# Optimization experiments

Measured on AMD Instinct MI355X. Metric: run time of the kernel, lower is better.

## Reference

```python
import jax, jax.numpy as jnp
import numpy as np

HID_DIM = 1024
B, S = 8, 2048
SCALE = float(np.sqrt(HID_DIM))
NEG = -1e10


def setup_inputs() -> dict:
    key = jax.random.key(0)
    ks = jax.random.split(key, 13)
    d = HID_DIM
    std = 1.0 / np.sqrt(d)
    return {
        "query": jax.random.normal(ks[0], (B, S, d), jnp.float32),
        "key_": jax.random.normal(ks[1], (B, S, d), jnp.float32),
        "value": jax.random.normal(ks[2], (B, S, d), jnp.float32),
        "mask": jax.random.randint(ks[3], (B, S), 0, 2, jnp.int32),
        "Wq": jax.random.uniform(ks[4], (d, d), jnp.float32, -std, std),
        "bq": jax.random.uniform(ks[5], (d,), jnp.float32, -std, std),
        "Wk": jax.random.uniform(ks[6], (d, d), jnp.float32, -std, std),
        "bk": jax.random.uniform(ks[7], (d,), jnp.float32, -std, std),
        "Wv": jax.random.uniform(ks[8], (d, d), jnp.float32, -std, std),
        "bv": jax.random.uniform(ks[9], (d,), jnp.float32, -std, std),
        "Wfc": jax.random.uniform(ks[10], (d, d), jnp.float32, -std, std),
        "bfc": jax.random.uniform(ks[11], (d,), jnp.float32, -std, std),
    }


def reference(query, key_, value, mask, Wq, bq, Wk, bk, Wv, bv, Wfc, bfc):
    # Linear projections (torch Linear: x @ W.T + b)
    Q = jnp.einsum("bsd,ed->bse", query, Wq) + bq
    K = jnp.einsum("bsd,ed->bse", key_, Wk) + bk
    V = jnp.einsum("bsd,ed->bse", value, Wv) + bv
    # Scaled dot-product energy: [B, S, S]
    energy = jnp.einsum("bqd,bkd->bqk", Q, K) / SCALE
    # Faithful to source: mask broadcast over last dim masks QUERY rows
    energy = jnp.where(mask[:, :, None] == 0, NEG, energy)
    attention = jax.nn.softmax(energy, axis=-1)  # dropout=0 (eval)
    x = jnp.einsum("bqk,bkd->bqd", attention, V)
    out = jnp.einsum("bsd,ed->bse", x, Wfc) + bfc
    return out
```

## Files before the change

kernel.cpp:

```cpp
#include <hip/hip_runtime.h>
#include <hip/hip_bf16.h>


#define DEVINL __device__ __forceinline__

typedef __bf16 bf16x8 __attribute__((ext_vector_type(8)));
typedef float f32x4 __attribute__((ext_vector_type(4)));

static constexpr int Bb = 8;
static constexpr int S = 2048;
static constexpr int D = 1024;

DEVINL unsigned short f32_to_bf16(float f) {
  unsigned u = __float_as_uint(f);
  u = (u + 0x7FFFu + ((u >> 16) & 1u)) >> 16;
  return (unsigned short)u;
}
DEVINL float bflo(unsigned u) { return __uint_as_float(u << 16); }
DEVINL float bfhi(unsigned u) { return __uint_as_float(u & 0xFFFF0000u); }

DEVINL void gload16(const unsigned short* g, char* l) {
  __builtin_amdgcn_global_load_lds((__attribute__((address_space(1))) void*)g,
                                   (__attribute__((address_space(3))) void*)l,
                                   16, 0, 0);
}
DEVINL void gload16u(const unsigned short* g, unsigned short* l) {
  gload16(g, (char*)l);
}

#define BAR() __builtin_amdgcn_s_barrier()
#define LGK0() asm volatile("s_waitcnt lgkmcnt(0)" ::: "memory")

#define PH_OPEN() \
  BAR();          \
  LGK0();         \
  __builtin_amdgcn_s_setprio(1)
#define PH_CLOSE()               \
  __builtin_amdgcn_s_setprio(0); \
  BAR()

#define MFMA_QUAD(A_, B_, MO, NO)                                              \
  {                                                                            \
    _Pragma("unroll") for (int mi_ = 0; mi_ < 4; mi_++) {                      \
      _Pragma("unroll") for (int nj_ = 0; nj_ < 2; nj_++) {                    \
        acc[(MO) + mi_][(NO) + nj_] = __builtin_amdgcn_mfma_f32_16x16x32_bf16( \
            A_[mi_][0], B_[nj_][0], acc[(MO) + mi_][(NO) + nj_], 0, 0, 0);     \
        acc[(MO) + mi_][(NO) + nj_] = __builtin_amdgcn_mfma_f32_16x16x32_bf16( \
            A_[mi_][1], B_[nj_][1], acc[(MO) + mi_][(NO) + nj_], 0, 0, 0);     \
      }                                                                        \
    }                                                                          \
  }

__global__ __launch_bounds__(256) void conv_f32_bf16(const float* __restrict__ in,
                                                     unsigned short* __restrict__ out,
                                                     int n8) {
  int i = blockIdx.x * 256 + threadIdx.x;
  int stride = gridDim.x * 256;
  for (; i < n8; i += stride) {
    const float4* p = (const float4*)in + (size_t)i * 2;
    float4 a = p[0], b = p[1];
    uint4 o;
    o.x = (unsigned)f32_to_bf16(a.x) | ((unsigned)f32_to_bf16(a.y) << 16);
    o.y = (unsigned)f32_to_bf16(a.z) | ((unsigned)f32_to_bf16(a.w) << 16);
    o.z = (unsigned)f32_to_bf16(b.x) | ((unsigned)f32_to_bf16(b.y) << 16);
    o.w = (unsigned)f32_to_bf16(b.z) | ((unsigned)f32_to_bf16(b.w) << 16);
    ((uint4*)out)[i] = o;
  }
}

__global__ __launch_bounds__(256) void tconv(const float* __restrict__ in,
                                             unsigned short* __restrict__ out,
                                             int R, int C) {
  __shared__ unsigned short t[64][72];
  const int c0 = blockIdx.x * 64, r0 = blockIdx.y * 64, b = blockIdx.z;
  in += (size_t)b * R * C;
  out += (size_t)b * R * C;
  const int tr = threadIdx.x >> 4;
  const int tc = threadIdx.x & 15;
#pragma unroll
  for (int i = 0; i < 4; i++) {
    int row = tr + i * 16;
    float4 v = *(const float4*)(in + (size_t)(r0 + row) * C + c0 + tc * 4);
    t[tc * 4 + 0][row] = f32_to_bf16(v.x);
    t[tc * 4 + 1][row] = f32_to_bf16(v.y);
    t[tc * 4 + 2][row] = f32_to_bf16(v.z);
    t[tc * 4 + 3][row] = f32_to_bf16(v.w);
  }
  __syncthreads();
  const int c = threadIdx.x >> 2, rs = (threadIdx.x & 3) * 16;
  unsigned short tmp[16];
#pragma unroll
  for (int j = 0; j < 16; j++) tmp[j] = t[c][rs + j];
  *(uint4*)(out + (size_t)(c0 + c) * R + r0 + rs) = *(const uint4*)&tmp[0];
  *(uint4*)(out + (size_t)(c0 + c) * R + r0 + rs + 8) = *(const uint4*)&tmp[8];
}

__global__ __launch_bounds__(256) void cvec_kernel(const float* __restrict__ Wfc,
                                                   const float* __restrict__ bv,
                                                   const float* __restrict__ bfc,
                                                   float* __restrict__ cv) {
  const int f = blockIdx.x;
  const float* row = Wfc + (size_t)f * 1024;
  float s = 0.f;
  for (int e = threadIdx.x; e < 1024; e += 256) s += row[e] * bv[e];
#pragma unroll
  for (int off = 32; off >= 1; off >>= 1) s += __shfl_xor(s, off);
  __shared__ float red[4];
  const int wave = threadIdx.x >> 6, lane = threadIdx.x & 63;
  if (lane == 0) red[wave] = s;
  __syncthreads();
  if (threadIdx.x == 0) cv[f] = red[0] + red[1] + red[2] + red[3] + bfc[f];
}

__global__ __launch_bounds__(256) void gvec_kernel(const unsigned short* __restrict__ WkT,
                                                   const float* __restrict__ bq,
                                                   float* __restrict__ g32) {
  const int e = blockIdx.x;
  const unsigned short* row = WkT + (size_t)e * 1024;
  const int j0 = threadIdx.x * 4;
  uint2 v = *(const uint2*)(row + j0);
  float4 b4 = *(const float4*)(bq + j0);
  float s = bflo(v.x) * b4.x + bfhi(v.x) * b4.y + bflo(v.y) * b4.z + bfhi(v.y) * b4.w;
#pragma unroll
  for (int off = 32; off >= 1; off >>= 1) s += __shfl_xor(s, off);
  __shared__ float red[4];
  const int wave = threadIdx.x >> 6, lane = threadIdx.x & 63;
  if (lane == 0) red[wave] = s;
  __syncthreads();
  if (threadIdx.x == 0) g32[e] = (red[0] + red[1] + red[2] + red[3]) * (1.0f / 32.0f);
}

__global__ __launch_bounds__(256) void wvec_kernel(const unsigned short* __restrict__ xk,
                                                   const float* __restrict__ g32,
                                                   float* __restrict__ w32) {
  const int row = blockIdx.x * 4 + (threadIdx.x >> 6);
  const int lane = threadIdx.x & 63;
  const unsigned short* r = xk + (size_t)row * 1024;
  float s = 0.f;
#pragma unroll
  for (int c = 0; c < 2; c++) {
    const int e0 = c * 512 + lane * 8;
    uint4 v = *(const uint4*)(r + e0);
    unsigned u[4] = {v.x, v.y, v.z, v.w};
#pragma unroll
    for (int i = 0; i < 4; i++) {
      float2 gg = *(const float2*)(g32 + e0 + i * 2);
      s += bflo(u[i]) * gg.x + bfhi(u[i]) * gg.y;
    }
  }
#pragma unroll
  for (int off = 32; off >= 1; off >>= 1) s += __shfl_xor(s, off);
  if (lane == 0) w32[row] = s;
}

__global__ __launch_bounds__(256) void rowinv_kernel(const float* __restrict__ partialT,
                                                     float* __restrict__ rowinv) {
  const int r = blockIdx.x * 256 + threadIdx.x;
  float s = 0.f;
#pragma unroll
  for (int c = 0; c < 16; c++) s += partialT[(size_t)c * 16384 + r];
  rowinv[r] = 1.0f / s;
}

__global__ __launch_bounds__(256) void gemm128(const unsigned short* __restrict__ A,
                                               const unsigned short* __restrict__ Bt,
                                               unsigned short* __restrict__ C,
                                               int M, int N, int K,
                                               long long bsA, long long bsB, long long bsC) {
  const int tid = threadIdx.x;
  const int wave = tid >> 6;
  const int lane = tid & 63;
  const int wr = wave >> 1, wc = wave & 1;
  const int m0 = blockIdx.y * 128, n0 = blockIdx.x * 128;
  A += (size_t)blockIdx.z * bsA;
  Bt += (size_t)blockIdx.z * bsB;
  C += (size_t)blockIdx.z * bsC;

  __shared__ unsigned short lds[2][2][128 * 32];

  const int srow = wave * 16 + (lane >> 2);
  const int scol = (lane & 3) * 8;
  const unsigned short* gA = A + (size_t)(m0 + srow) * K + scol;
  const unsigned short* gB = Bt + (size_t)(n0 + srow) * K + scol;

  f32x4 acc[4][4];
#pragma unroll
  for (int i = 0; i < 4; i++)
#pragma unroll
    for (int j = 0; j < 4; j++) acc[i][j] = (f32x4){0.f, 0.f, 0.f, 0.f};

  const int nk = K >> 5;
  auto stage = [&](int buf, int kt) {
    const unsigned short* a0 = gA + (size_t)kt * 32;
    const unsigned short* b0 = gB + (size_t)kt * 32;
    unsigned short* la = &lds[buf][0][wave * 512];
    unsigned short* lb = &lds[buf][1][wave * 512];
    gload16u(a0, la);
    gload16u(a0 + (size_t)64 * K, la + 2048);
    gload16u(b0, lb);
    gload16u(b0 + (size_t)64 * K, lb + 2048);
  };

  stage(0, 0);
  asm volatile("s_waitcnt vmcnt(0)" ::: "memory");
  __syncthreads();

  const int fm = lane & 15;
  const int fk = (lane >> 4) * 8;

  int cur = 0;
  for (int t = 0; t < nk; ++t) {
    if (t + 1 < nk) stage(cur ^ 1, t + 1);
    bf16x8 af[4], bfr[4];
#pragma unroll
    for (int i = 0; i < 4; i++)
      af[i] = *(const bf16x8*)&lds[cur][0][(wr * 64 + i * 16 + fm) * 32 + fk];
#pragma unroll
    for (int j = 0; j < 4; j++)
      bfr[j] = *(const bf16x8*)&lds[cur][1][(wc * 64 + j * 16 + fm) * 32 + fk];
#pragma unroll
    for (int i = 0; i < 4; i++)
#pragma unroll
      for (int j = 0; j < 4; j++)
        acc[i][j] = __builtin_amdgcn_mfma_f32_16x16x32_bf16(af[i], bfr[j], acc[i][j], 0, 0, 0);
    asm volatile("s_waitcnt vmcnt(0)" ::: "memory");
    __syncthreads();
    cur ^= 1;
  }

  const int en = n0 + wc * 64 + fm;
  const int em = m0 + wr * 64 + ((lane >> 4) << 2);
#pragma unroll
  for (int j = 0; j < 4; j++)
#pragma unroll
    for (int i = 0; i < 4; i++)
#pragma unroll
      for (int r = 0; r < 4; r++)
        C[(size_t)(em + i * 16 + r) * N + en + j * 16] = f32_to_bf16(acc[i][j][r]);
}

template <int OUTMODE, bool HAS_BIAS>
__global__ __launch_bounds__(512, 2) void gemm256(
    const unsigned short* __restrict__ A, const unsigned short* __restrict__ Bt,
    const float* __restrict__ bias, const int* __restrict__ msk,
    float* __restrict__ partial, void* __restrict__ Cv,
    int M, int N, int K, long long bsA, long long bsB, long long bsC,
    float scale) {
  extern __shared__ char smem[];
  const int tid = threadIdx.x;
  const int wave = tid >> 6, lane = tid & 63;
  const int wr = wave >> 2, wc = wave & 3;

  const int gx = gridDim.x, gy = gridDim.y;
  const int nwg = gx * gy * (int)gridDim.z;
  const int wg = blockIdx.x + gx * (blockIdx.y + gy * blockIdx.z);
  const int swz = (wg & 7) * (nwg >> 3) + (wg >> 3);
  const int bx = swz % gx;
  const int rem = swz / gx;
  const int by = rem % gy;
  const int bz = rem / gy;

  const int m0 = by * 256, n0 = bx * 256;
  A += (size_t)bz * bsA;
  Bt += (size_t)bz * bsB;

  const int rl = lane >> 3;
  const int gl = (lane & 7) ^ rl;
  const unsigned short* gA = A + (size_t)(m0 + wave * 8 + rl) * K + gl * 8;
  const unsigned short* gB = Bt + (size_t)(n0 + wave * 8 + rl) * K + gl * 8;

  auto stageA = [&](int db, int t, int h) {
    const unsigned short* g = gA + (size_t)(h * 128) * K + (size_t)t * 64;
    char* l = smem + db * 65536 + h * 16384 + wave * 1024;
    gload16(g, l);
    gload16(g + (size_t)64 * K, l + 8192);
  };
  auto stageB = [&](int db, int t, int h) {
    const unsigned short* g = gB + (size_t)(h * 128) * K + (size_t)t * 64;
    char* l = smem + db * 65536 + 32768 + h * 16384 + wave * 1024;
    gload16(g, l);
    gload16(g + (size_t)64 * K, l + 8192);
  };

  const int fr = lane & 15;
  const int fg = lane >> 4;
  auto readA = [&](int db, int mi, int kc) -> bf16x8 {
    const int row = wr * 128 + mi * 16 + fr;
    const int g = (kc * 4 + fg) ^ (row & 7);
    return *(const bf16x8*)(smem + db * 65536 + row * 128 + g * 16);
  };
  auto readB = [&](int db, int nj, int kc) -> bf16x8 {
    const int row = wc * 64 + nj * 16 + fr;
    const int g = (kc * 4 + fg) ^ (row & 7);
    return *(const bf16x8*)(smem + db * 65536 + 32768 + row * 128 + g * 16);
  };

  f32x4 acc[8][4];
#pragma unroll
  for (int i = 0; i < 8; i++)
#pragma unroll
    for (int j = 0; j < 4; j++) acc[i][j] = (f32x4){0.f, 0.f, 0.f, 0.f};

  stageA(0, 0, 0);
  stageA(0, 0, 1);
  stageB(0, 0, 0);
  stageB(0, 0, 1);
  stageB(1, 1, 0);
  stageB(1, 1, 1);
  asm volatile("s_waitcnt vmcnt(4)" ::: "memory");
  BAR();

  const int nt = K >> 6;
  const int niter = nt >> 1;

  for (int j = 0; j < niter; ++j) {
    const int t0 = 2 * j, t1 = 2 * j + 1;
    const bool more = (j + 1 < niter);
    bf16x8 a[4][2], b0[2][2], b1[2][2];

#pragma unroll
    for (int mi = 0; mi < 4; mi++) { a[mi][0] = readA(0, mi, 0); a[mi][1] = readA(0, mi, 1); }
#pragma unroll
    for (int nj = 0; nj < 2; nj++) { b0[nj][0] = readB(0, nj, 0); b0[nj][1] = readB(0, nj, 1); }
    stageA(1, t1, 0);
    asm volatile("s_waitcnt lgkmcnt(8)" ::: "memory");
    PH_OPEN();
    MFMA_QUAD(a, b0, 0, 0);
    PH_CLOSE();

#pragma unroll
    for (int nj = 0; nj < 2; nj++) { b1[nj][0] = readB(0, nj + 2, 0); b1[nj][1] = readB(0, nj + 2, 1); }
    stageA(1, t1, 1);
    PH_OPEN();
    MFMA_QUAD(a, b1, 0, 2);
    PH_CLOSE();

#pragma unroll
    for (int mi = 0; mi < 4; mi++) { a[mi][0] = readA(0, mi + 4, 0); a[mi][1] = readA(0, mi + 4, 1); }
    if (more) stageB(0, t0 + 2, 0);
    PH_OPEN();
    MFMA_QUAD(a, b0, 4, 0);
    PH_CLOSE();

    if (more) stageB(0, t0 + 2, 1);
    BAR();
    __builtin_amdgcn_s_setprio(1);
    MFMA_QUAD(a, b1, 4, 2);
    __builtin_amdgcn_s_setprio(0);
    if (more)
      asm volatile("s_waitcnt vmcnt(4)" ::: "memory");
    else
      asm volatile("s_waitcnt vmcnt(0)" ::: "memory");
    BAR();

#pragma unroll
    for (int mi = 0; mi < 4; mi++) { a[mi][0] = readA(1, mi, 0); a[mi][1] = readA(1, mi, 1); }
#pragma unroll
    for (int nj = 0; nj < 2; nj++) { b0[nj][0] = readB(1, nj, 0); b0[nj][1] = readB(1, nj, 1); }
    if (more) stageA(0, t0 + 2, 0);
    asm volatile("s_waitcnt lgkmcnt(8)" ::: "memory");
    PH_OPEN();
    MFMA_QUAD(a, b0, 0, 0);
    PH_CLOSE();

#pragma unroll
    for (int nj = 0; nj < 2; nj++) { b1[nj][0] = readB(1, nj + 2, 0); b1[nj][1] = readB(1, nj + 2, 1); }
    if (more) stageA(0, t0 + 2, 1);
    PH_OPEN();
    MFMA_QUAD(a, b1, 0, 2);
    PH_CLOSE();

#pragma unroll
    for (int mi = 0; mi < 4; mi++) { a[mi][0] = readA(1, mi + 4, 0); a[mi][1] = readA(1, mi + 4, 1); }
    if (more) stageB(1, t1 + 2, 0);
    PH_OPEN();
    MFMA_QUAD(a, b0, 4, 0);
    PH_CLOSE();

    if (more) stageB(1, t1 + 2, 1);
    BAR();
    __builtin_amdgcn_s_setprio(1);
    MFMA_QUAD(a, b1, 4, 2);
    __builtin_amdgcn_s_setprio(0);
    asm volatile("s_waitcnt vmcnt(4)" ::: "memory");
    BAR();
  }

  const int row0base = m0 + wr * 128 + fg * 4;
  const int colbase = n0 + wc * 64 + fr;

  if (OUTMODE == 0) {
    float* C = (float*)Cv + (size_t)bz * bsC;
#pragma unroll
    for (int nj = 0; nj < 4; nj++) {
      const int col = colbase + nj * 16;
      const float bv = HAS_BIAS ? bias[col] : 0.0f;
#pragma unroll
      for (int mi = 0; mi < 8; mi++) {
        const int row = row0base + mi * 16;
#pragma unroll
        for (int r = 0; r < 4; r++)
          C[(size_t)(row + r) * N + col] = acc[mi][nj][r] + bv;
      }
    }
  } else {
    const int lcol = wc * 64 + fr;
    const int lrow0 = wr * 128 + fg * 4;
    int mk[4];
    float ri[4];
    float psum[4] = {0.f, 0.f, 0.f, 0.f};
    if (OUTMODE == 3) {
#pragma unroll
      for (int nj = 0; nj < 4; nj++) mk[nj] = msk[bz * 2048 + colbase + nj * 16];
    }
    if (OUTMODE == 4) {
#pragma unroll
      for (int nj = 0; nj < 4; nj++) ri[nj] = partial[bz * 2048 + colbase + nj * 16];
    }
#pragma unroll
    for (int mi = 0; mi < 8; mi++) {
      const int lrow = lrow0 + mi * 16;
      float4 w4 = make_float4(0.f, 0.f, 0.f, 0.f);
      if (OUTMODE == 3) w4 = *(const float4*)&bias[bz * 2048 + row0base + mi * 16];
#pragma unroll
      for (int nj = 0; nj < 4; nj++) {
        float v0, v1, v2, v3;
        if (OUTMODE == 3) {
          v0 = mk[nj] ? __expf(fmaf(acc[mi][nj][0], scale, w4.x)) : 1.0f;
          v1 = mk[nj] ? __expf(fmaf(acc[mi][nj][1], scale, w4.y)) : 1.0f;
          v2 = mk[nj] ? __expf(fmaf(acc[mi][nj][2], scale, w4.z)) : 1.0f;
          v3 = mk[nj] ? __expf(fmaf(acc[mi][nj][3], scale, w4.w)) : 1.0f;
          psum[nj] += (v0 + v1) + (v2 + v3);
        } else if (OUTMODE == 4) {
          v0 = acc[mi][nj][0] * ri[nj];
          v1 = acc[mi][nj][1] * ri[nj];
          v2 = acc[mi][nj][2] * ri[nj];
          v3 = acc[mi][nj][3] * ri[nj];
        } else {
          v0 = acc[mi][nj][0];
          v1 = acc[mi][nj][1];
          v2 = acc[mi][nj][2];
          v3 = acc[mi][nj][3];
        }
        unsigned lo = (unsigned)f32_to_bf16(v0) | ((unsigned)f32_to_bf16(v1) << 16);
        unsigned hi = (unsigned)f32_to_bf16(v2) | ((unsigned)f32_to_bf16(v3) << 16);
        const int c = lcol + nj * 16;
        const int byte = c * 512 + ((((lrow >> 3) ^ (c & 7)) << 4) | ((lrow & 4) << 1));
        *(uint2*)(smem + byte) = make_uint2(lo, hi);
      }
    }
    if (OUTMODE == 3) {
#pragma unroll
      for (int nj = 0; nj < 4; nj++) {
        psum[nj] += __shfl_xor(psum[nj], 16);
        psum[nj] += __shfl_xor(psum[nj], 32);
      }
      if (fg == 0) {
#pragma unroll
        for (int nj = 0; nj < 4; nj++)
          partial[(size_t)(by * 2 + wr) * 16384 + bz * 2048 + colbase + nj * 16] = psum[nj];
      }
    }
    __syncthreads();
    unsigned short* C = (unsigned short*)Cv + (size_t)bz * bsC;
    const int qh = wave * 2 + (lane >> 5);
    const int kl = (lane & 31) * 8;
#pragma unroll
    for (int p = 0; p < 16; p++) {
      const int ql = qh + p * 16;
      const int byte = ql * 512 + ((((kl >> 3) ^ (ql & 7)) << 4));
      uint4 vv = *(const uint4*)(smem + byte);
      *(uint4*)(C + (size_t)(n0 + ql) * M + m0 + kl) = vv;
    }
  }
}

extern "C" void kernel_launch(void* const* d_in, const int* in_sizes, int n_in,
                              void* d_out, int out_size, void* d_ws, size_t ws_size,
                              hipStream_t stream) {
  const float* q = (const float*)d_in[0];
  const float* k_ = (const float*)d_in[1];
  const float* v = (const float*)d_in[2];
  const int* msk = (const int*)d_in[3];
  const float* Wq = (const float*)d_in[4];
  const float* bq = (const float*)d_in[5];
  const float* Wk = (const float*)d_in[6];
  const float* Wv = (const float*)d_in[8];
  const float* bv = (const float*)d_in[9];
  const float* Wfc = (const float*)d_in[10];
  const float* bfc = (const float*)d_in[11];

  char* ws = (char*)d_ws;
  const size_t MB = 1u << 20;
  unsigned short* WkT = (unsigned short*)(ws + 0 * MB);
  unsigned short* WfcB = (unsigned short*)(ws + 2 * MB);
  unsigned short* WqT = (unsigned short*)(ws + 4 * MB);
  unsigned short* WvT = (unsigned short*)(ws + 6 * MB);
  unsigned short* Mt = (unsigned short*)(ws + 8 * MB);
  unsigned short* W2 = (unsigned short*)(ws + 10 * MB);
  float* partialT = (float*)(ws + 12 * MB);
  float* rowinv = (float*)(ws + 13 * MB);
  float* cv = (float*)(ws + 13 * MB + 256 * 1024);
  float* g32 = (float*)(ws + 13 * MB + 512 * 1024);
  float* w32 = (float*)(ws + 13 * MB + 768 * 1024);
  unsigned short* Qm = (unsigned short*)(ws + 16 * MB);
  unsigned short* xkB = (unsigned short*)(ws + 48 * MB);
  unsigned short* valueT = (unsigned short*)(ws + 80 * MB);
  unsigned short* xqB = (unsigned short*)(ws + 112 * MB);
  unsigned short* E = (unsigned short*)(ws + 112 * MB);
  unsigned short* y = Qm;

  const int NBS = Bb * S * D;

  auto conv = [&](const float* in, unsigned short* out, int n) {
    int n8 = n / 8;
    int blocks = (n8 + 255) / 256;
    if (blocks > 2048) blocks = 2048;
    conv_f32_bf16<<<dim3(blocks), dim3(256), 0, stream>>>(in, out, n8);
  };

  tconv<<<dim3(16, 16, 1), dim3(256), 0, stream>>>(Wq, WqT, D, D);
  tconv<<<dim3(16, 16, 1), dim3(256), 0, stream>>>(Wk, WkT, D, D);
  conv(Wfc, WfcB, D * D);
  tconv<<<dim3(16, 16, 1), dim3(256), 0, stream>>>(Wv, WvT, D, D);
  gemm128<<<dim3(8, 8, 2), dim3(256), 0, stream>>>(
      WkT, WqT, Mt, D, D, D, (long long)D * D, (long long)D * D, (long long)D * D);
  cvec_kernel<<<dim3(1024), dim3(256), 0, stream>>>(Wfc, bv, bfc, cv);
  gvec_kernel<<<dim3(1024), dim3(256), 0, stream>>>(WkT, bq, g32);

  const float invscale = 1.0f / 32.0f;

  conv(q, xqB, NBS);
  gemm256<1, false><<<dim3(64, 4, 1), dim3(512), 131072, stream>>>(
      Mt, xqB, nullptr, nullptr, nullptr, Qm, D, Bb * S, D, 0, 0, 0, 1.0f);
  conv(k_, xkB, NBS);
  wvec_kernel<<<dim3(4096), dim3(256), 0, stream>>>(xkB, g32, w32);
  tconv<<<dim3(16, 32, 8), dim3(256), 0, stream>>>(v, valueT, S, D);
  gemm256<3, false><<<dim3(8, 8, 8), dim3(512), 131072, stream>>>(
      xkB, Qm, w32, msk, partialT, E, S, S, D, (long long)S * D,
      (long long)S * D, (long long)S * S, invscale);
  rowinv_kernel<<<dim3(64), dim3(256), 0, stream>>>(partialT, rowinv);
  gemm256<4, false><<<dim3(8, 4, 8), dim3(512), 131072, stream>>>(
      valueT, E, nullptr, nullptr, rowinv, y, D, S, S, (long long)D * S,
      (long long)S * S, (long long)S * D, 1.0f);
  gemm256<0, true><<<dim3(4, 64, 1), dim3(512), 131072, stream>>>(
      y, W2, cv, nullptr, nullptr, d_out, Bb * S, D, D, 0, 0, 0, 1.0f);
}
```

Measured before the change: 325.5 us.

## Reassociate attention output: project V through Wfc first, fuse normalization into final GEMM

Instead of computing attention·V and then applying the output projection, V is projected by the combined Wv·Wfc weight first, and the final GEMM multiplies E by the projected V with the row normalization and bias folded into its epilogue. This drops the separate value transpose kernel and one intermediate pass over the B×S×D activation, and gives the GEMM separate lda/ldb strides. The A-tile prefetch is also moved earlier so both A halves load alongside B, with a deeper vmcnt wait. The risks are extra in-flight loads and register pressure, plus changed bf16 rounding from the new association order.

```diff
diff --git a/kernel.cpp b/kernel.cpp
--- a/kernel.cpp
+++ b/kernel.cpp
@@ -244,8 +244,8 @@
     const unsigned short* __restrict__ A, const unsigned short* __restrict__ Bt,
     const float* __restrict__ bias, const int* __restrict__ msk,
     float* __restrict__ partial, void* __restrict__ Cv,
-    int M, int N, int K, long long bsA, long long bsB, long long bsC,
-    float scale) {
+    int M, int N, int K, int lda, int ldb,
+    long long bsA, long long bsB, long long bsC, float scale) {
   extern __shared__ char smem[];
   const int tid = threadIdx.x;
   const int wave = tid >> 6, lane = tid & 63;
@@ -266,20 +266,20 @@
 
   const int rl = lane >> 3;
   const int gl = (lane & 7) ^ rl;
-  const unsigned short* gA = A + (size_t)(m0 + wave * 8 + rl) * K + gl * 8;
-  const unsigned short* gB = Bt + (size_t)(n0 + wave * 8 + rl) * K + gl * 8;
+  const unsigned short* gA = A + (size_t)(m0 + wave * 8 + rl) * lda + gl * 8;
+  const unsigned short* gB = Bt + (size_t)(n0 + wave * 8 + rl) * ldb + gl * 8;
 
   auto stageA = [&](int db, int t, int h) {
-    const unsigned short* g = gA + (size_t)(h * 128) * K + (size_t)t * 64;
+    const unsigned short* g = gA + (size_t)(h * 128) * lda + (size_t)t * 64;
     char* l = smem + db * 65536 + h * 16384 + wave * 1024;
     gload16(g, l);
-    gload16(g + (size_t)64 * K, l + 8192);
+    gload16(g + (size_t)64 * lda, l + 8192);
   };
   auto stageB = [&](int db, int t, int h) {
-    const unsigned short* g = gB + (size_t)(h * 128) * K + (size_t)t * 64;
+    const unsigned short* g = gB + (size_t)(h * 128) * ldb + (size_t)t * 64;
     char* l = smem + db * 65536 + 32768 + h * 16384 + wave * 1024;
     gload16(g, l);
-    gload16(g + (size_t)64 * K, l + 8192);
+    gload16(g + (size_t)64 * ldb, l + 8192);
   };
 
   const int fr = lane & 15;
@@ -307,7 +307,9 @@
   stageB(0, 0, 1);
   stageB(1, 1, 0);
   stageB(1, 1, 1);
-  asm volatile("s_waitcnt vmcnt(4)" ::: "memory");
+  stageA(1, 1, 0);
+  stageA(1, 1, 1);
+  asm volatile("s_waitcnt vmcnt(8)" ::: "memory");
   BAR();
 
   const int nt = K >> 6;
@@ -322,7 +324,6 @@
     for (int mi = 0; mi < 4; mi++) { a[mi][0] = readA(0, mi, 0); a[mi][1] = readA(0, mi, 1); }
 #pragma unroll
     for (int nj = 0; nj < 2; nj++) { b0[nj][0] = readB(0, nj, 0); b0[nj][1] = readB(0, nj, 1); }
-    stageA(1, t1, 0);
     asm volatile("s_waitcnt lgkmcnt(8)" ::: "memory");
     PH_OPEN();
     MFMA_QUAD(a, b0, 0, 0);
@@ -330,7 +331,6 @@
 
 #pragma unroll
     for (int nj = 0; nj < 2; nj++) { b1[nj][0] = readB(0, nj + 2, 0); b1[nj][1] = readB(0, nj + 2, 1); }
-    stageA(1, t1, 1);
     PH_OPEN();
     MFMA_QUAD(a, b1, 0, 2);
     PH_CLOSE();
@@ -342,13 +342,17 @@
     MFMA_QUAD(a, b0, 4, 0);
     PH_CLOSE();
 
-    if (more) stageB(0, t0 + 2, 1);
+    if (more) {
+      stageB(0, t0 + 2, 1);
+      stageA(0, t0 + 2, 0);
+      stageA(0, t0 + 2, 1);
+    }
     BAR();
     __builtin_amdgcn_s_setprio(1);
     MFMA_QUAD(a, b1, 4, 2);
     __builtin_amdgcn_s_setprio(0);
     if (more)
-      asm volatile("s_waitcnt vmcnt(4)" ::: "memory");
+      asm volatile("s_waitcnt vmcnt(8)" ::: "memory");
     else
       asm volatile("s_waitcnt vmcnt(0)" ::: "memory");
     BAR();
@@ -357,7 +361,6 @@
     for (int mi = 0; mi < 4; mi++) { a[mi][0] = readA(1, mi, 0); a[mi][1] = readA(1, mi, 1); }
 #pragma unroll
     for (int nj = 0; nj < 2; nj++) { b0[nj][0] = readB(1, nj, 0); b0[nj][1] = readB(1, nj, 1); }
-    if (more) stageA(0, t0 + 2, 0);
     asm volatile("s_waitcnt lgkmcnt(8)" ::: "memory");
     PH_OPEN();
     MFMA_QUAD(a, b0, 0, 0);
@@ -365,7 +368,6 @@
 
 #pragma unroll
     for (int nj = 0; nj < 2; nj++) { b1[nj][0] = readB(1, nj + 2, 0); b1[nj][1] = readB(1, nj + 2, 1); }
-    if (more) stageA(0, t0 + 2, 1);
     PH_OPEN();
     MFMA_QUAD(a, b1, 0, 2);
     PH_CLOSE();
@@ -377,45 +379,49 @@
     MFMA_QUAD(a, b0, 4, 0);
     PH_CLOSE();
 
-    if (more) stageB(1, t1 + 2, 1);
+    if (more) {
+      stageB(1, t1 + 2, 1);
+      stageA(1, t1 + 2, 0);
+      stageA(1, t1 + 2, 1);
+    }
     BAR();
     __builtin_amdgcn_s_setprio(1);
     MFMA_QUAD(a, b1, 4, 2);
     __builtin_amdgcn_s_setprio(0);
-    asm volatile("s_waitcnt vmcnt(4)" ::: "memory");
+    if (more)
+      asm volatile("s_waitcnt vmcnt(8)" ::: "memory");
+    else
+      asm volatile("s_waitcnt vmcnt(0)" ::: "memory");
     BAR();
   }
 
   const int row0base = m0 + wr * 128 + fg * 4;
   const int colbase = n0 + wc * 64 + fr;
 
-  if (OUTMODE == 0) {
+  if (OUTMODE == 6) {
     float* C = (float*)Cv + (size_t)bz * bsC;
 #pragma unroll
-    for (int nj = 0; nj < 4; nj++) {
-      const int col = colbase + nj * 16;
-      const float bv = HAS_BIAS ? bias[col] : 0.0f;
-#pragma unroll
-      for (int mi = 0; mi < 8; mi++) {
-        const int row = row0base + mi * 16;
-#pragma unroll
-        for (int r = 0; r < 4; r++)
-          C[(size_t)(row + r) * N + col] = acc[mi][nj][r] + bv;
+    for (int mi = 0; mi < 8; mi++) {
+      const int j0 = row0base + mi * 16;
+      const float4 ri = *(const float4*)&partial[bz * 2048 + j0];
+#pragma unroll
+      for (int nj = 0; nj < 4; nj++) {
+        const int col = colbase + nj * 16;
+        const float cvv = HAS_BIAS ? bias[col] : 0.0f;
+        C[(size_t)(j0 + 0) * N + col] = fmaf(acc[mi][nj][0], ri.x, cvv);
+        C[(size_t)(j0 + 1) * N + col] = fmaf(acc[mi][nj][1], ri.y, cvv);
+        C[(size_t)(j0 + 2) * N + col] = fmaf(acc[mi][nj][2], ri.z, cvv);
+        C[(size_t)(j0 + 3) * N + col] = fmaf(acc[mi][nj][3], ri.w, cvv);
       }
     }
   } else {
     const int lcol = wc * 64 + fr;
     const int lrow0 = wr * 128 + fg * 4;
     int mk[4];
-    float ri[4];
     float psum[4] = {0.f, 0.f, 0.f, 0.f};
     if (OUTMODE == 3) {
 #pragma unroll
       for (int nj = 0; nj < 4; nj++) mk[nj] = msk[bz * 2048 + colbase + nj * 16];
-    }
-    if (OUTMODE == 4) {
-#pragma unroll
-      for (int nj = 0; nj < 4; nj++) ri[nj] = partial[bz * 2048 + colbase + nj * 16];
     }
 #pragma unroll
     for (int mi = 0; mi < 8; mi++) {
@@ -431,11 +437,6 @@
           v2 = mk[nj] ? __expf(fmaf(acc[mi][nj][2], scale, w4.z)) : 1.0f;
           v3 = mk[nj] ? __expf(fmaf(acc[mi][nj][3], scale, w4.w)) : 1.0f;
           psum[nj] += (v0 + v1) + (v2 + v3);
-        } else if (OUTMODE == 4) {
-          v0 = acc[mi][nj][0] * ri[nj];
-          v1 = acc[mi][nj][1] * ri[nj];
-          v2 = acc[mi][nj][2] * ri[nj];
-          v3 = acc[mi][nj][3] * ri[nj];
         } else {
           v0 = acc[mi][nj][0];
           v1 = acc[mi][nj][1];
@@ -503,12 +504,12 @@
   float* cv = (float*)(ws + 13 * MB + 256 * 1024);
   float* g32 = (float*)(ws + 13 * MB + 512 * 1024);
   float* w32 = (float*)(ws + 13 * MB + 768 * 1024);
-  unsigned short* Qm = (unsigned short*)(ws + 16 * MB);
+  unsigned short* Qc = (unsigned short*)(ws + 16 * MB);
   unsigned short* xkB = (unsigned short*)(ws + 48 * MB);
-  unsigned short* valueT = (unsigned short*)(ws + 80 * MB);
+  unsigned short* vpT = (unsigned short*)(ws + 80 * MB);
   unsigned short* xqB = (unsigned short*)(ws + 112 * MB);
+  unsigned short* vB = (unsigned short*)(ws + 144 * MB);
   unsigned short* E = (unsigned short*)(ws + 112 * MB);
-  unsigned short* y = Qm;
 
   const int NBS = Bb * S * D;
 
@@ -532,17 +533,17 @@
 
   conv(q, xqB, NBS);
   gemm256<1, false><<<dim3(64, 4, 1), dim3(512), 131072, stream>>>(
-      Mt, xqB, nullptr, nullptr, nullptr, Qm, D, Bb * S, D, 0, 0, 0, 1.0f);
+      Mt, xqB, nullptr, nullptr, nullptr, Qc, D, Bb * S, D, D, D, 0, 0, 0, 1.0f);
   conv(k_, xkB, NBS);
   wvec_kernel<<<dim3(4096), dim3(256), 0, stream>>>(xkB, g32, w32);
-  tconv<<<dim3(16, 32, 8), dim3(256), 0, stream>>>(v, valueT, S, D);
+  conv(v, vB, NBS);
+  gemm256<1, false><<<dim3(4, 64, 1), dim3(512), 131072, stream>>>(
+      vB, W2, nullptr, nullptr, nullptr, vpT, Bb * S, D, D, D, D, 0, 0, 0, 1.0f);
   gemm256<3, false><<<dim3(8, 8, 8), dim3(512), 131072, stream>>>(
-      xkB, Qm, w32, msk, partialT, E, S, S, D, (long long)S * D,
-      (long long)S * D, (long long)S * S, invscale);
+      xkB, Qc, w32, msk, partialT, E, S, S, D, D, D,
+      (long long)S * D, (long long)S * D, (long long)S * S, invscale);
   rowinv_kernel<<<dim3(64), dim3(256), 0, stream>>>(partialT, rowinv);
-  gemm256<4, false><<<dim3(8, 4, 8), dim3(512), 131072, stream>>>(
-      valueT, E, nullptr, nullptr, rowinv, y, D, S, S, (long long)D * S,
-      (long long)S * S, (long long)S * D, 1.0f);
-  gemm256<0, true><<<dim3(4, 64, 1), dim3(512), 131072, stream>>>(
-      y, W2, cv, nullptr, nullptr, d_out, Bb * S, D, D, 0, 0, 0, 1.0f);
-}
+  gemm256<6, true><<<dim3(4, 8, 8), dim3(512), 131072, stream>>>(
+      E, vpT, cv, nullptr, rowinv, d_out, S, D, S, S, Bb * S,
+      (long long)S * S, (long long)S, (long long)S * D, 1.0f);
+}
```

Result: no change. 328.2 us (+0.8%).
